# Kernel optimization log

Measured on AMD Instinct MI355X. Metric: run time of the kernel, lower is better.

## Reference

```python
import jax, jax.numpy as jnp
import numpy as np

B, S, D = 4, 2048, 1024
H = 8  # hardcoded in AttentionLayer
HD = D // H
FF = 4096
EPS = 1e-5


def _layernorm(x):
    # LayerNorm(hidden_dim, elementwise_affine=False), eps=1e-5
    mu = jnp.mean(x, axis=-1, keepdims=True)
    var = jnp.var(x, axis=-1, keepdims=True)
    return (x - mu) / jnp.sqrt(var + EPS)


def setup_inputs() -> dict:
    key = jax.random.key(0)
    ks = jax.random.split(key, 5)
    scale = 0.02
    return {
        "x": jax.random.normal(ks[0], (B, S, D), dtype=jnp.float32),
        "qkv_proj": jax.random.normal(ks[1], (D, 3 * D), dtype=jnp.float32) * scale,
        "o_proj": jax.random.normal(ks[2], (D, D), dtype=jnp.float32) * scale,
        "ff1": jax.random.normal(ks[3], (D, FF), dtype=jnp.float32) * scale,
        "ff2": jax.random.normal(ks[4], (FF, D), dtype=jnp.float32) * scale,
    }


def reference(x, qkv_proj, o_proj, ff1, ff2):
    b, s, d = x.shape
    # --- attention ---
    qkv = jnp.matmul(x, qkv_proj)                       # [b,s,3d]
    qkv = qkv.reshape(b, s, H, 3 * HD).transpose(0, 2, 1, 3)  # [b,h,s,3hd]
    q, k, v = jnp.split(qkv, 3, axis=-1)                # each [b,h,s,hd]
    logits = jnp.einsum('bhqd,bhkd->bhqk', q, k) / jnp.sqrt(jnp.float32(HD))
    attn = jax.nn.softmax(logits, axis=-1)
    vals = jnp.einsum('bhqk,bhkd->bhqd', attn, v)       # [b,h,s,hd]
    vals = vals.transpose(0, 2, 1, 3).reshape(b, s, d)
    attn_out = jnp.matmul(vals, o_proj)
    # --- residual + norm + FFN + residual + norm ---
    x = _layernorm(x + attn_out)
    ff_out = jnp.matmul(jax.nn.relu(jnp.matmul(x, ff1)), ff2)
    x = _layernorm(x + ff_out)
    return x
```

## Files before the change

### kernel.cpp

```cpp
#include <hip/hip_runtime.h>
#include <hip/hip_bf16.h>


typedef float floatx4 __attribute__((ext_vector_type(4)));
typedef float floatx16 __attribute__((ext_vector_type(16)));
typedef short bf16x8 __attribute__((ext_vector_type(8)));

#define DEVI __device__ __forceinline__

typedef const __attribute__((address_space(1))) unsigned int* gas1_t;
typedef __attribute__((address_space(3))) unsigned int* las3_t;

DEVI void gll16(const void* g, void* l) {
  __builtin_amdgcn_global_load_lds((gas1_t)g, (las3_t)l, 16, 0, 0);
}

DEVI short bfbits(float f) {
  __hip_bfloat16 h = __float2bfloat16(f);
  return *reinterpret_cast<short*>(&h);
}

template<int EPI, int SPLITK>
__global__ __launch_bounds__(256, 4) void gemm_bt(
    const __hip_bfloat16* __restrict__ A,
    const __hip_bfloat16* __restrict__ BT,
    float* __restrict__ Cf, float* __restrict__ Cf2,
    __hip_bfloat16* __restrict__ Cb,
    int M, int N, int K)
{
  __shared__ __hip_bfloat16 As[128 * 64];
  __shared__ __hip_bfloat16 Bs[128 * 64];
  const int tid = threadIdx.x;
  const int wave = tid >> 6, lane = tid & 63;
  const int lane15 = lane & 15, quad = lane >> 4;
  const int row0 = blockIdx.x * 128, col0 = blockIdx.y * 128;
  const int wr = (wave >> 1) * 64, wc = (wave & 1) * 64;
  const int Kh = K / SPLITK;
  const size_t kofs = (SPLITK > 1) ? (size_t)blockIdx.z * Kh : 0;

  floatx4 acc[4][4] = {};

  const int srow = tid >> 3;
  const int sblk = (tid & 7) ^ (srow & 7);
  const __hip_bfloat16* Ag = A + (size_t)(row0 + srow) * K + kofs + sblk * 8;
  const __hip_bfloat16* Bg = BT + (size_t)(col0 + srow) * K + kofs + sblk * 8;
  char* Asl = (char*)As + tid * 16;
  char* Bsl = (char*)Bs + tid * 16;
  const size_t rstep = (size_t)32 * K;

  const int x7 = lane15 & 7;
  for (int k0 = 0; k0 < Kh; k0 += 64) {
    __syncthreads();
#pragma unroll
    for (int p = 0; p < 4; p++) {
      gll16(Ag + k0 + p * rstep, Asl + p * 4096);
      gll16(Bg + k0 + p * rstep, Bsl + p * 4096);
    }
    __syncthreads();
#pragma unroll
    for (int kc = 0; kc < 2; kc++) {
      bf16x8 af[4], bb[4];
#pragma unroll
      for (int t = 0; t < 4; t++) {
        const int r = wr + t * 16 + lane15;
        af[t] = *(const bf16x8*)((const char*)As + r * 128 + (((kc * 4 + quad) ^ x7) << 4));
      }
#pragma unroll
      for (int t = 0; t < 4; t++) {
        const int r = wc + t * 16 + lane15;
        bb[t] = *(const bf16x8*)((const char*)Bs + r * 128 + (((kc * 4 + quad) ^ x7) << 4));
      }
#pragma unroll
      for (int i = 0; i < 4; i++)
#pragma unroll
        for (int j = 0; j < 4; j++)
          acc[i][j] = __builtin_amdgcn_mfma_f32_16x16x32_bf16(af[i], bb[j], acc[i][j], 0, 0, 0);
    }
  }

  float* Cp = (SPLITK > 1 && blockIdx.z) ? Cf2 : Cf;
#pragma unroll
  for (int i = 0; i < 4; i++) {
    const int mb = row0 + wr + i * 16 + quad * 4;
#pragma unroll
    for (int j = 0; j < 4; j++) {
      const int n = col0 + wc + j * 16 + lane15;
#pragma unroll
      for (int r = 0; r < 4; r++) {
        const size_t idx = (size_t)(mb + r) * N + n;
        const float v = acc[i][j][r];
        if (EPI == 0) {
          Cb[idx] = __float2bfloat16(v);
        } else if (EPI == 2) {
          Cb[idx] = __float2bfloat16(v > 0.f ? v : 0.f);
        } else {
          Cp[idx] = v;
        }
      }
    }
  }
}

__global__ __launch_bounds__(256, 2) void attn_kernel(
    const __hip_bfloat16* __restrict__ qkv,
    const __hip_bfloat16* __restrict__ Vt,
    __hip_bfloat16* __restrict__ vals)
{
  __shared__ __hip_bfloat16 Ak[128 * 128];
  __shared__ __hip_bfloat16 Bq[128 * 128];

  const int tid = threadIdx.x;
  const int wave = tid >> 6, lane = tid & 63;
  const int l31 = lane & 31, l5 = lane >> 5;
  const int qt = blockIdx.x, bh = blockIdx.y;
  const int b = bh >> 3, h = bh & 7;
  const size_t tokbase = (size_t)b * 2048;
  const float scale = 0.08838834764831845f;

  const int sw8 = ((tid & 15) ^ (tid >> 4)) * 8;
  const int srow = tid >> 4;
  const __hip_bfloat16* qg  = qkv + (tokbase + qt * 128) * 3072 + h * 384 + sw8;
  const __hip_bfloat16* kg0 = qkv + tokbase * 3072 + h * 384 + 128 + sw8;
  const __hip_bfloat16* vg0 = Vt + (size_t)bh * 128 * 2048 + sw8;

#pragma unroll
  for (int rd = 0; rd < 8; rd++)
    gll16(qg + (size_t)(rd * 16 + srow) * 3072, (char*)Bq + rd * 4096 + tid * 16);
  __syncthreads();

  const int rx = l31 & 15;
  bf16x8 qf[8];
  {
    const char* qb = (const char*)Bq + (wave * 32 + l31) * 256;
#pragma unroll
    for (int ks = 0; ks < 8; ks++)
      qf[ks] = *(const bf16x8*)(qb + (((ks * 2 + l5) ^ rx) << 4));
  }
#pragma unroll
  for (int rd = 0; rd < 8; rd++)
    gll16(kg0 + (size_t)(rd * 16 + srow) * 3072, (char*)Ak + rd * 4096 + tid * 16);
  __syncthreads();

  floatx16 oacc[4] = {};
  float lsum = 0.f;

  for (int kt = 0; kt < 16; kt++) {
    if (kt) __syncthreads();

#pragma unroll
    for (int rd = 0; rd < 8; rd++)
      gll16(vg0 + (size_t)kt * 128 + (size_t)(rd * 16 + srow) * 2048,
            (char*)Bq + rd * 4096 + tid * 16);

    floatx16 sacc[4] = {};
#pragma unroll
    for (int ks = 0; ks < 8; ks++) {
      const int off = ((ks * 2 + l5) ^ rx) << 4;
      const char* kb = (const char*)Ak + l31 * 256 + off;
#pragma unroll
      for (int nt = 0; nt < 4; nt++) {
        const bf16x8 ak = *(const bf16x8*)(kb + nt * 8192);
        sacc[nt] = __builtin_amdgcn_mfma_f32_32x32x16_bf16(ak, qf[ks], sacc[nt], 0, 0, 0);
      }
    }

    unsigned int pk0[16], pk1[16];
#pragma unroll
    for (int idx = 0; idx < 16; idx++) {
      const int nt = idx >> 2, g4 = (idx & 3) * 4;
      const float p0 = __expf(sacc[nt][g4 + 0] * scale);
      const float p1 = __expf(sacc[nt][g4 + 1] * scale);
      const float p2 = __expf(sacc[nt][g4 + 2] * scale);
      const float p3 = __expf(sacc[nt][g4 + 3] * scale);
      lsum += (p0 + p1) + (p2 + p3);
      pk0[idx] = (unsigned int)(unsigned short)bfbits(p0) |
                 ((unsigned int)(unsigned short)bfbits(p1) << 16);
      pk1[idx] = (unsigned int)(unsigned short)bfbits(p2) |
                 ((unsigned int)(unsigned short)bfbits(p3) << 16);
    }
    bf16x8 pf[8];
#pragma unroll
    for (int ks = 0; ks < 8; ks++) {
      const unsigned int own0 = l5 ? pk0[ks * 2 + 1] : pk0[ks * 2];
      const unsigned int own1 = l5 ? pk1[ks * 2 + 1] : pk1[ks * 2];
      const unsigned int snd0 = l5 ? pk0[ks * 2] : pk0[ks * 2 + 1];
      const unsigned int snd1 = l5 ? pk1[ks * 2] : pk1[ks * 2 + 1];
      const unsigned int rc0 = (unsigned int)__shfl_xor((int)snd0, 32);
      const unsigned int rc1 = (unsigned int)__shfl_xor((int)snd1, 32);
      union { int4 i; bf16x8 v; } u;
      u.i.x = l5 ? (int)rc0 : (int)own0;
      u.i.y = l5 ? (int)rc1 : (int)own1;
      u.i.z = l5 ? (int)own0 : (int)rc0;
      u.i.w = l5 ? (int)own1 : (int)rc1;
      pf[ks] = u.v;
    }

    __syncthreads();
    if (kt < 15) {
#pragma unroll
      for (int rd = 0; rd < 8; rd++)
        gll16(kg0 + (size_t)((kt + 1) * 128 + rd * 16 + srow) * 3072,
              (char*)Ak + rd * 4096 + tid * 16);
    }

#pragma unroll
    for (int ks = 0; ks < 8; ks++) {
      const int off = ((ks * 2 + l5) ^ rx) << 4;
      const char* vb = (const char*)Bq + l31 * 256 + off;
#pragma unroll
      for (int nt = 0; nt < 4; nt++) {
        const bf16x8 av = *(const bf16x8*)(vb + nt * 8192);
        oacc[nt] = __builtin_amdgcn_mfma_f32_32x32x16_bf16(av, pf[ks], oacc[nt], 0, 0, 0);
      }
    }
  }

  lsum += __shfl_xor(lsum, 32);
  const float linv = 1.f / lsum;

  const size_t row = tokbase + (size_t)qt * 128 + wave * 32 + l31;
  __hip_bfloat16* vrow = vals + row * 1024 + h * 128 + 4 * l5;
#pragma unroll
  for (int nt = 0; nt < 4; nt++)
#pragma unroll
    for (int g = 0; g < 4; g++) {
      short4 sv;
      sv.x = bfbits(oacc[nt][g * 4 + 0] * linv);
      sv.y = bfbits(oacc[nt][g * 4 + 1] * linv);
      sv.z = bfbits(oacc[nt][g * 4 + 2] * linv);
      sv.w = bfbits(oacc[nt][g * 4 + 3] * linv);
      *(short4*)(vrow + nt * 32 + g * 8) = sv;
    }
}

__global__ __launch_bounds__(256) void cvt_bf16_k(const float* __restrict__ in,
                                                  __hip_bfloat16* __restrict__ out) {
  const size_t i = (size_t)blockIdx.x * 256 + threadIdx.x;
  const float4 v = ((const float4*)in)[i];
  short4 sv;
  sv.x = bfbits(v.x); sv.y = bfbits(v.y); sv.z = bfbits(v.z); sv.w = bfbits(v.w);
  ((short4*)out)[i] = sv;
}

__global__ __launch_bounds__(256) void wtrans_k(const float* __restrict__ W,
                                                __hip_bfloat16* __restrict__ WT,
                                                int K, int N) {
  __shared__ float t[32][33];
  const int tx = threadIdx.x & 31, ty = threadIdx.x >> 5;
  const int n0 = blockIdx.x * 32, k0 = blockIdx.y * 32;
#pragma unroll
  for (int i = 0; i < 4; i++)
    t[ty + i * 8][tx] = W[(size_t)(k0 + ty + i * 8) * N + n0 + tx];
  __syncthreads();
#pragma unroll
  for (int i = 0; i < 4; i++)
    WT[(size_t)(n0 + ty + i * 8) * K + k0 + tx] = __float2bfloat16(t[tx][ty + i * 8]);
}

__global__ __launch_bounds__(256) void vtrans_k(const __hip_bfloat16* __restrict__ qkv,
                                                __hip_bfloat16* __restrict__ Vt) {
  __shared__ __hip_bfloat16 t[32][33];
  const int tx = threadIdx.x & 31, ty = threadIdx.x >> 5;
  const int s0 = blockIdx.x * 32, d0 = blockIdx.y * 32, bh = blockIdx.z;
  const int b = bh >> 3, h = bh & 7;
#pragma unroll
  for (int i = 0; i < 4; i++)
    t[ty + i * 8][tx] = qkv[((size_t)b * 2048 + s0 + ty + i * 8) * 3072 + h * 384 + 256 + d0 + tx];
  __syncthreads();
#pragma unroll
  for (int i = 0; i < 4; i++)
    Vt[((size_t)bh * 128 + d0 + ty + i * 8) * 2048 + s0 + tx] = t[tx][ty + i * 8];
}

template<bool RES_BF16, bool FINAL>
__global__ __launch_bounds__(256) void ln_red_k(
    const float* __restrict__ p0, const float* __restrict__ p1,
    const float* __restrict__ resf, const __hip_bfloat16* __restrict__ resb,
    __hip_bfloat16* __restrict__ ob, float* __restrict__ of) {
  const int row = blockIdx.x, tid = threadIdx.x;
  const size_t base = (size_t)row * 1024;
  const float4 a = ((const float4*)(p0 + base))[tid];
  const float4 bb = ((const float4*)(p1 + base))[tid];
  float4 v;
  if (RES_BF16) {
    const short4 rb = ((const short4*)(resb + base))[tid];
    v.x = a.x + bb.x + __bfloat162float(*(const __hip_bfloat16*)&rb.x);
    v.y = a.y + bb.y + __bfloat162float(*(const __hip_bfloat16*)&rb.y);
    v.z = a.z + bb.z + __bfloat162float(*(const __hip_bfloat16*)&rb.z);
    v.w = a.w + bb.w + __bfloat162float(*(const __hip_bfloat16*)&rb.w);
  } else {
    const float4 rf = ((const float4*)(resf + base))[tid];
    v.x = a.x + bb.x + rf.x; v.y = a.y + bb.y + rf.y;
    v.z = a.z + bb.z + rf.z; v.w = a.w + bb.w + rf.w;
  }
  float s = v.x + v.y + v.z + v.w;
  float q = v.x * v.x + v.y * v.y + v.z * v.z + v.w * v.w;
#pragma unroll
  for (int off = 32; off; off >>= 1) { s += __shfl_xor(s, off); q += __shfl_xor(q, off); }
  __shared__ float ss[4], sq[4];
  const int wave = tid >> 6;
  if ((tid & 63) == 0) { ss[wave] = s; sq[wave] = q; }
  __syncthreads();
  s = ss[0] + ss[1] + ss[2] + ss[3];
  q = sq[0] + sq[1] + sq[2] + sq[3];
  const float mean = s * (1.f / 1024.f);
  const float var = q * (1.f / 1024.f) - mean * mean;
  const float rstd = rsqrtf(var + 1e-5f);
  float4 o;
  o.x = (v.x - mean) * rstd; o.y = (v.y - mean) * rstd;
  o.z = (v.z - mean) * rstd; o.w = (v.w - mean) * rstd;
  if (FINAL) {
    ((float4*)(of + base))[tid] = o;
  } else {
    short4 sv;
    sv.x = bfbits(o.x); sv.y = bfbits(o.y); sv.z = bfbits(o.z); sv.w = bfbits(o.w);
    ((short4*)(ob + base))[tid] = sv;
  }
}

extern "C" void kernel_launch(void* const* d_in, const int* in_sizes, int n_in,
                              void* d_out, int out_size, void* d_ws, size_t ws_size,
                              hipStream_t stream) {
  const float* x    = (const float*)d_in[0];
  const float* qkvw = (const float*)d_in[1];
  const float* ow   = (const float*)d_in[2];
  const float* f1   = (const float*)d_in[3];
  const float* f2   = (const float*)d_in[4];
  float* out = (float*)d_out;

  char* ws = (char*)d_ws;
  const size_t MB = 1024 * 1024;
  __hip_bfloat16* xb   = (__hip_bfloat16*)(ws);
  __hip_bfloat16* vals = xb;
  float*          P1f  = (float*)(ws);
  __hip_bfloat16* qkvT = (__hip_bfloat16*)(ws + 16 * MB);
  __hip_bfloat16* oT   = (__hip_bfloat16*)(ws + 22 * MB);
  __hip_bfloat16* f1T  = (__hip_bfloat16*)(ws + 24 * MB);
  __hip_bfloat16* f2T  = (__hip_bfloat16*)(ws + 32 * MB);
  __hip_bfloat16* qkvb = (__hip_bfloat16*)(ws + 40 * MB);
  __hip_bfloat16* Vt   = (__hip_bfloat16*)(ws + 88 * MB);
  float*          P0o  = (float*)(ws + 40 * MB);
  float*          P1o  = (float*)(ws + 72 * MB);
  __hip_bfloat16* hmid = (__hip_bfloat16*)(ws + 40 * MB);
  float*          P0f  = (float*)(ws + 104 * MB);
  __hip_bfloat16* x1b  = (__hip_bfloat16*)(ws + 136 * MB);
  (void)in_sizes; (void)n_in; (void)out_size; (void)ws_size;

  cvt_bf16_k<<<8192, 256, 0, stream>>>(x, xb);
  wtrans_k<<<dim3(96, 32), 256, 0, stream>>>(qkvw, qkvT, 1024, 3072);
  wtrans_k<<<dim3(32, 32), 256, 0, stream>>>(ow, oT, 1024, 1024);
  wtrans_k<<<dim3(128, 32), 256, 0, stream>>>(f1, f1T, 1024, 4096);
  wtrans_k<<<dim3(32, 128), 256, 0, stream>>>(f2, f2T, 4096, 1024);
  gemm_bt<0, 1><<<dim3(64, 24, 1), 256, 0, stream>>>(xb, qkvT, nullptr, nullptr,
                                                     qkvb, 8192, 3072, 1024);
  vtrans_k<<<dim3(64, 4, 32), 256, 0, stream>>>(qkvb, Vt);
  attn_kernel<<<dim3(16, 32), 256, 0, stream>>>(qkvb, Vt, vals);
  gemm_bt<4, 2><<<dim3(64, 8, 2), 256, 0, stream>>>(vals, oT, P0o, P1o,
                                                    nullptr, 8192, 1024, 1024);
  ln_red_k<false, false><<<8192, 256, 0, stream>>>(P0o, P1o, x, nullptr, x1b, nullptr);
  gemm_bt<2, 1><<<dim3(64, 32, 1), 256, 0, stream>>>(x1b, f1T, nullptr, nullptr,
                                                     hmid, 8192, 4096, 1024);
  gemm_bt<4, 2><<<dim3(64, 8, 2), 256, 0, stream>>>(hmid, f2T, P0f, P1f,
                                                    nullptr, 8192, 1024, 4096);
  ln_red_k<true, true><<<8192, 256, 0, stream>>>(P0f, P1f, nullptr, x1b, nullptr, out);
}
```

Measured before the change: 500.6 us.

## Fuse prep kernels, cheapen bf16 packing, swap attention grid order

Merges the input conversion and four weight transposes into one launch with block-range dispatch, which removes several kernel launches and their gaps. In the attention kernel, bf16 packing now uses a single byte-permute with an add-0x8000 bias, a round-half-up approximation instead of the full round-to-nearest-even conversion. The attention grid is reordered so heads vary fastest, which changes which blocks share K/V in cache. Rounding differs slightly from before and NaN handling is dropped in the new packing path.

```diff
diff --git a/kernel.cpp b/kernel.cpp
--- a/kernel.cpp
+++ b/kernel.cpp
@@ -18,6 +18,12 @@
 DEVI short bfbits(float f) {
   __hip_bfloat16 h = __float2bfloat16(f);
   return *reinterpret_cast<short*>(&h);
+}
+
+DEVI unsigned int packbf(float lo, float hi) {
+  return __builtin_amdgcn_perm(__float_as_uint(hi) + 0x8000u,
+                               __float_as_uint(lo) + 0x8000u,
+                               0x07060302u);
 }
 
 template<int EPI, int SPLITK>
@@ -112,7 +118,7 @@
   const int tid = threadIdx.x;
   const int wave = tid >> 6, lane = tid & 63;
   const int l31 = lane & 31, l5 = lane >> 5;
-  const int qt = blockIdx.x, bh = blockIdx.y;
+  const int bh = blockIdx.x, qt = blockIdx.y;
   const int b = bh >> 3, h = bh & 7;
   const size_t tokbase = (size_t)b * 2048;
   const float scale = 0.08838834764831845f;
@@ -173,10 +179,8 @@
       const float p2 = __expf(sacc[nt][g4 + 2] * scale);
       const float p3 = __expf(sacc[nt][g4 + 3] * scale);
       lsum += (p0 + p1) + (p2 + p3);
-      pk0[idx] = (unsigned int)(unsigned short)bfbits(p0) |
-                 ((unsigned int)(unsigned short)bfbits(p1) << 16);
-      pk1[idx] = (unsigned int)(unsigned short)bfbits(p2) |
-                 ((unsigned int)(unsigned short)bfbits(p3) << 16);
+      pk0[idx] = packbf(p0, p1);
+      pk1[idx] = packbf(p2, p3);
     }
     bf16x8 pf[8];
 #pragma unroll
@@ -224,37 +228,45 @@
   for (int nt = 0; nt < 4; nt++)
 #pragma unroll
     for (int g = 0; g < 4; g++) {
-      short4 sv;
-      sv.x = bfbits(oacc[nt][g * 4 + 0] * linv);
-      sv.y = bfbits(oacc[nt][g * 4 + 1] * linv);
-      sv.z = bfbits(oacc[nt][g * 4 + 2] * linv);
-      sv.w = bfbits(oacc[nt][g * 4 + 3] * linv);
-      *(short4*)(vrow + nt * 32 + g * 8) = sv;
-    }
-}
-
-__global__ __launch_bounds__(256) void cvt_bf16_k(const float* __restrict__ in,
-                                                  __hip_bfloat16* __restrict__ out) {
-  const size_t i = (size_t)blockIdx.x * 256 + threadIdx.x;
-  const float4 v = ((const float4*)in)[i];
-  short4 sv;
-  sv.x = bfbits(v.x); sv.y = bfbits(v.y); sv.z = bfbits(v.z); sv.w = bfbits(v.w);
-  ((short4*)out)[i] = sv;
-}
-
-__global__ __launch_bounds__(256) void wtrans_k(const float* __restrict__ W,
-                                                __hip_bfloat16* __restrict__ WT,
-                                                int K, int N) {
-  __shared__ float t[32][33];
+      uint2 pk;
+      pk.x = packbf(oacc[nt][g * 4 + 0] * linv, oacc[nt][g * 4 + 1] * linv);
+      pk.y = packbf(oacc[nt][g * 4 + 2] * linv, oacc[nt][g * 4 + 3] * linv);
+      *(uint2*)(vrow + nt * 32 + g * 8) = pk;
+    }
+}
+
+__global__ __launch_bounds__(256) void prep_k(
+    const float* __restrict__ x, __hip_bfloat16* __restrict__ xb,
+    const float* __restrict__ qkvw, __hip_bfloat16* __restrict__ qkvT,
+    const float* __restrict__ ow, __hip_bfloat16* __restrict__ oT,
+    const float* __restrict__ f1, __hip_bfloat16* __restrict__ f1T,
+    const float* __restrict__ f2, __hip_bfloat16* __restrict__ f2T)
+{
+  const int bid = blockIdx.x;
+  if (bid < 8192) {
+    const size_t i = (size_t)bid * 256 + threadIdx.x;
+    const float4 v = ((const float4*)x)[i];
+    short4 sv;
+    sv.x = bfbits(v.x); sv.y = bfbits(v.y); sv.z = bfbits(v.z); sv.w = bfbits(v.w);
+    ((short4*)xb)[i] = sv;
+    return;
+  }
+  int t = bid - 8192;
+  const float* W; __hip_bfloat16* WT; int K, N, nbx;
+  if (t < 3072) { W = qkvw; WT = qkvT; K = 1024; N = 3072; nbx = 96; }
+  else if (t < 3072 + 1024) { t -= 3072; W = ow; WT = oT; K = 1024; N = 1024; nbx = 32; }
+  else if (t < 3072 + 1024 + 4096) { t -= 3072 + 1024; W = f1; WT = f1T; K = 1024; N = 4096; nbx = 128; }
+  else { t -= 3072 + 1024 + 4096; W = f2; WT = f2T; K = 4096; N = 1024; nbx = 32; }
+  __shared__ float tl[32][33];
   const int tx = threadIdx.x & 31, ty = threadIdx.x >> 5;
-  const int n0 = blockIdx.x * 32, k0 = blockIdx.y * 32;
+  const int n0 = (t % nbx) * 32, k0 = (t / nbx) * 32;
 #pragma unroll
   for (int i = 0; i < 4; i++)
-    t[ty + i * 8][tx] = W[(size_t)(k0 + ty + i * 8) * N + n0 + tx];
+    tl[ty + i * 8][tx] = W[(size_t)(k0 + ty + i * 8) * N + n0 + tx];
   __syncthreads();
 #pragma unroll
   for (int i = 0; i < 4; i++)
-    WT[(size_t)(n0 + ty + i * 8) * K + k0 + tx] = __float2bfloat16(t[tx][ty + i * 8]);
+    WT[(size_t)(n0 + ty + i * 8) * K + k0 + tx] = __float2bfloat16(tl[tx][ty + i * 8]);
 }
 
 __global__ __launch_bounds__(256) void vtrans_k(const __hip_bfloat16* __restrict__ qkv,
@@ -346,15 +358,11 @@
   __hip_bfloat16* x1b  = (__hip_bfloat16*)(ws + 136 * MB);
   (void)in_sizes; (void)n_in; (void)out_size; (void)ws_size;
 
-  cvt_bf16_k<<<8192, 256, 0, stream>>>(x, xb);
-  wtrans_k<<<dim3(96, 32), 256, 0, stream>>>(qkvw, qkvT, 1024, 3072);
-  wtrans_k<<<dim3(32, 32), 256, 0, stream>>>(ow, oT, 1024, 1024);
-  wtrans_k<<<dim3(128, 32), 256, 0, stream>>>(f1, f1T, 1024, 4096);
-  wtrans_k<<<dim3(32, 128), 256, 0, stream>>>(f2, f2T, 4096, 1024);
+  prep_k<<<20480, 256, 0, stream>>>(x, xb, qkvw, qkvT, ow, oT, f1, f1T, f2, f2T);
   gemm_bt<0, 1><<<dim3(64, 24, 1), 256, 0, stream>>>(xb, qkvT, nullptr, nullptr,
                                                      qkvb, 8192, 3072, 1024);
   vtrans_k<<<dim3(64, 4, 32), 256, 0, stream>>>(qkvb, Vt);
-  attn_kernel<<<dim3(16, 32), 256, 0, stream>>>(qkvb, Vt, vals);
+  attn_kernel<<<dim3(32, 16), 256, 0, stream>>>(qkvb, Vt, vals);
   gemm_bt<4, 2><<<dim3(64, 8, 2), 256, 0, stream>>>(vals, oT, P0o, P1o,
                                                     nullptr, 8192, 1024, 1024);
   ln_red_k<false, false><<<8192, 256, 0, stream>>>(P0o, P1o, x, nullptr, x1b, nullptr);
```

New measurement: 456.2 us. 1.1x faster.
